# Optimization experiments

Hardware: AMD Instinct MI355X
Metric: run time of the kernel (lower is better)

Reference implementation:

```python
import jax, jax.numpy as jnp
import numpy as np
import math

NH, NKV, HD = 8, 1, 128
SOFTCAP = 30.0
ROPE_BASE = 500000.0


def _rope_tables(T, hd, base):
    half = hd // 2
    inv_freq = 1.0 / (base ** (np.arange(half, dtype=np.float32) / half))
    t = np.arange(T, dtype=np.float32)
    ang = np.outer(t, inv_freq)  # [T, half]
    return jnp.asarray(np.cos(ang)), jnp.asarray(np.sin(ang))


def apply_rope(x, cos, sin):
    # x: [B, T, H, hd]; cos/sin: [T, hd//2]
    half = x.shape[-1] // 2
    x1, x2 = x[..., :half], x[..., half:]
    T = x.shape[1]
    c = cos[:T][None, :, None, :]
    s = sin[:T][None, :, None, :]
    return jnp.concatenate([x1 * c - x2 * s, x1 * s + x2 * c], axis=-1)


def setup_inputs() -> dict:
    key = jax.random.key(0)
    ks = jax.random.split(key, 5)
    B, T, D = 4, 2048, 1024
    KD = NKV * HD
    x = jax.random.normal(ks[0], (B, T, D), dtype=jnp.float32)
    Wq = jax.random.normal(ks[1], (D, D), dtype=jnp.float32) * (D ** -0.5)
    Wk = jax.random.normal(ks[2], (KD, D), dtype=jnp.float32) * (D ** -0.5)
    Wv = jax.random.normal(ks[3], (KD, D), dtype=jnp.float32) * (D ** -0.5)
    Wo = jax.random.normal(ks[4], (D, D), dtype=jnp.float32) * (D ** -0.5)
    qk_gain = jnp.full((NH,), 1.5, dtype=jnp.float32)  # qk_gain_init
    cos, sin = _rope_tables(T, HD, ROPE_BASE)
    return {"x": x, "Wq": Wq, "Wk": Wk, "Wv": Wv, "Wo": Wo,
            "qk_gain": qk_gain, "cos": cos, "sin": sin}


def reference(x, Wq, Wk, Wv, Wo, qk_gain, cos, sin):
    B, T, D = x.shape
    # projections (QuantLinear with qat disabled == plain linear, no bias)
    q = (x @ Wq.T).reshape(B, T, NH, HD)
    k = (x @ Wk.T).reshape(B, T, NKV, HD)
    v = (x @ Wv.T).reshape(B, T, NKV, HD)
    q = apply_rope(q, cos, sin)
    k = apply_rope(k, cos, sin)
    # learned per-head QK gain applied to queries
    q = q * qk_gain[None, None, :, 1 - 1][..., None] if False else q * qk_gain[None, None, :, None]
    # GQA: broadcast the single kv head across NH query heads
    scale = 1.0 / math.sqrt(HD)
    scores = jnp.einsum('bqhd,bkgd->bhqk', q, k) * scale  # g==NKV==1 broadcast
    # logit softcap before masking/softmax
    scores = SOFTCAP * jnp.tanh(scores / SOFTCAP)
    causal = jnp.tril(jnp.ones((T, T), dtype=bool))
    scores = jnp.where(causal[None, None], scores, -jnp.inf)
    attn = jax.nn.softmax(scores, axis=-1)  # [B, NH, T, T]
    out = jnp.einsum('bhqk,bkgd->bqhd', attn, v).reshape(B, T, NH * HD)
    return out @ Wo.T
```

## Files before the change

### kernel.cpp

```cpp
#include <hip/hip_runtime.h>
#include <hip/hip_bf16.h>

#define B_ 4
#define T_ 2048
#define D_ 1024
#define NH_ 8
#define HD_ 128

typedef short short8 __attribute__((ext_vector_type(8)));
typedef float floatx4 __attribute__((ext_vector_type(4)));

#if __has_builtin(__builtin_amdgcn_exp2f)
#define EXP2F __builtin_amdgcn_exp2f
#else
#define EXP2F exp2f
#endif
#if __has_builtin(__builtin_amdgcn_rcpf)
#define RCPF __builtin_amdgcn_rcpf
#else
__device__ __forceinline__ float RCPF(float x) { return 1.f / x; }
#endif

#if __has_builtin(__builtin_amdgcn_global_load_lds)
#define G2L(gp, lp)                                                        \
  __builtin_amdgcn_global_load_lds(                                        \
      (const __attribute__((address_space(1))) unsigned int*)(gp),         \
      (__attribute__((address_space(3))) unsigned int*)(lp), 16, 0, 0)
#else
#define G2L(gp, lp) (*(uint4*)(lp) = *(const uint4*)(gp))
#endif

__device__ __forceinline__ unsigned short f2b(float f) {
  union { float fl; unsigned int i; } v; v.fl = f;
  unsigned int r = v.i + 0x7fffu + ((v.i >> 16) & 1u);
  return (unsigned short)(r >> 16);
}
__device__ __forceinline__ unsigned int pack_bf16(float a, float b) {
  unsigned int ua = __float_as_uint(a) + 0x8000u;
  unsigned int ub = __float_as_uint(b) + 0x8000u;
  return (ua >> 16) | (ub & 0xffff0000u);
}
__device__ __forceinline__ float blo(unsigned int u) { return __uint_as_float(u << 16); }
__device__ __forceinline__ float bhi(unsigned int u) { return __uint_as_float(u & 0xffff0000u); }

__global__ __launch_bounds__(256) void cvt_kernel(
    const float* __restrict__ x,  const float* __restrict__ wq,
    const float* __restrict__ wk, const float* __restrict__ wv,
    const float* __restrict__ wo, unsigned short* __restrict__ dst)
{
  size_t i = ((size_t)blockIdx.x * 256 + threadIdx.x) * 8;
  const float* src; size_t off;
  if      (i <  8388608u) { src = x;  off = i; }
  else if (i <  9437184u) { src = wq; off = i - 8388608u; }
  else if (i <  9568256u) { src = wk; off = i - 9437184u; }
  else if (i <  9699328u) { src = wv; off = i - 9568256u; }
  else                    { src = wo; off = i - 9699328u; }
  float4 a = *(const float4*)(src + off);
  float4 b = *(const float4*)(src + off + 4);
  uint4 o;
  o.x = pack_bf16(a.x, a.y); o.y = pack_bf16(a.z, a.w);
  o.z = pack_bf16(b.x, b.y); o.w = pack_bf16(b.z, b.w);
  *(uint4*)(dst + i) = o;
}

template <bool C_F32>
__device__ __forceinline__ void gemm_body_1024(
    const unsigned short* __restrict__ Arow0,
    const unsigned short* __restrict__ Btile,
    void* __restrict__ Cb, int ldC)
{
  __shared__ unsigned short As[128 * 32];
  __shared__ unsigned short Bs[128 * 32];
  const int tid = threadIdx.x;
  const int lane = tid & 63;
  const int w = tid >> 6;
  const int wr = w >> 1, wc = w & 1;
  const int l15 = lane & 15, quad = lane >> 4;

  const unsigned short* a_src = Arow0 + (size_t)(tid >> 2) * 1024 + (tid & 3) * 8;
  const unsigned short* b_src = Btile + (size_t)(tid >> 2) * 1024 + (tid & 3) * 8;
  unsigned short* a_dst = &As[(tid >> 2) * 32 + (tid & 3) * 8];
  unsigned short* b_dst = &Bs[(tid >> 2) * 32 + (tid & 3) * 8];

  floatx4 zero = {0.f, 0.f, 0.f, 0.f};
  floatx4 acc[4][4];
#pragma unroll
  for (int i = 0; i < 4; i++)
#pragma unroll
    for (int j = 0; j < 4; j++) acc[i][j] = zero;

  for (int k0 = 0; k0 < 1024; k0 += 32) {
    __syncthreads();
    G2L(a_src + k0,         a_dst);
    G2L(a_src + 65536 + k0, a_dst + 2048);
    G2L(b_src + k0,         b_dst);
    G2L(b_src + 65536 + k0, b_dst + 2048);
    __syncthreads();
    short8 af[4], bfr[4];
#pragma unroll
    for (int i = 0; i < 4; i++)
      af[i] = *(const short8*)&As[(wr * 64 + i * 16 + l15) * 32 + quad * 8];
#pragma unroll
    for (int j = 0; j < 4; j++)
      bfr[j] = *(const short8*)&Bs[(wc * 64 + j * 16 + l15) * 32 + quad * 8];
#pragma unroll
    for (int i = 0; i < 4; i++)
#pragma unroll
      for (int j = 0; j < 4; j++)
        acc[i][j] = __builtin_amdgcn_mfma_f32_16x16x32_bf16(af[i], bfr[j], acc[i][j], 0, 0, 0);
  }
#pragma unroll
  for (int i = 0; i < 4; i++)
#pragma unroll
    for (int j = 0; j < 4; j++)
#pragma unroll
      for (int r = 0; r < 4; r++) {
        size_t off = (size_t)(wr * 64 + i * 16 + quad * 4 + r) * ldC + wc * 64 + j * 16 + l15;
        if (C_F32) ((float*)Cb)[off] = acc[i][j][r];
        else ((unsigned short*)Cb)[off] = f2b(acc[i][j][r]);
      }
}

__global__ __launch_bounds__(256) void gemm_qkv_kernel(
    const unsigned short* __restrict__ x,
    const unsigned short* __restrict__ Wq,
    const unsigned short* __restrict__ Wk,
    const unsigned short* __restrict__ Wv,
    unsigned short* __restrict__ q,
    unsigned short* __restrict__ k,
    unsigned short* __restrict__ v)
{
  const int bx = blockIdx.x, by = blockIdx.y;
  const unsigned short* Btile;
  unsigned short* C;
  int ldC, col0;
  if (by < 8) { Btile = Wq + (size_t)by * 128 * 1024; C = q; ldC = 1024; col0 = by * 128; }
  else if (by == 8) { Btile = Wk; C = k; ldC = 128; col0 = 0; }
  else { Btile = Wv; C = v; ldC = 128; col0 = 0; }
  gemm_body_1024<false>(x + (size_t)bx * 128 * 1024, Btile,
                        C + (size_t)bx * 128 * ldC + col0, ldC);
}

__global__ __launch_bounds__(256) void gemm_out_kernel(
    const unsigned short* __restrict__ ao,
    const unsigned short* __restrict__ Wo,
    float* __restrict__ out)
{
  const int bx = blockIdx.x, by = blockIdx.y;
  gemm_body_1024<true>(ao + (size_t)bx * 128 * 1024, Wo + (size_t)by * 128 * 1024,
                       out + (size_t)bx * 128 * 1024 + by * 128, 1024);
}

__global__ __launch_bounds__(256) void prep_kernel(
    unsigned short* __restrict__ q,
    unsigned short* __restrict__ k,
    const unsigned short* __restrict__ v,
    unsigned short* __restrict__ vT,
    const float* __restrict__ cosT,
    const float* __restrict__ sinT,
    const float* __restrict__ gain)
{
  __shared__ unsigned short tile[32 * 136];
  const int tid = threadIdx.x;
  if (blockIdx.x < 256) {
    const int b = blockIdx.x >> 6, t0 = (blockIdx.x & 63) * 32;
    for (int u = tid; u < 512; u += 256) {
      int r = u >> 4, c = u & 15;
      *(uint4*)&tile[r * 136 + c * 8] =
          *(const uint4*)(v + ((size_t)(b * T_ + t0 + r)) * 128 + c * 8);
    }
    __syncthreads();
    for (int u = tid; u < 512; u += 256) {
      int d = u >> 2, c = u & 3;
      short8 val;
#pragma unroll
      for (int j = 0; j < 8; j++) val[j] = (short)tile[(c * 8 + j) * 136 + d];
      *(short8*)(vT + ((size_t)(b * 128 + d)) * T_ + t0 + c * 8) = val;
    }
    return;
  }
  int idx = (blockIdx.x - 256) * 256 + tid;
  unsigned short* ptr;
  size_t base;
  int t, j;
  float g;
  if (idx < 524288) {
    j = idx & 7;
    int h = (idx >> 3) & 7;
    int bt = idx >> 6;
    t = bt & (T_ - 1);
    base = (size_t)bt * 1024 + h * 128 + j * 8;
    ptr = q;
    g = gain[h] * 0.0029462782549439484f;
  } else {
    int id = idx - 524288;
    j = id & 7;
    int bt = id >> 3;
    t = bt & (T_ - 1);
    base = (size_t)bt * 128 + j * 8;
    ptr = k;
    g = 1.f;
  }
  float4 ca = *(const float4*)&cosT[t * 64 + j * 8];
  float4 cb = *(const float4*)&cosT[t * 64 + j * 8 + 4];
  float4 sa = *(const float4*)&sinT[t * 64 + j * 8];
  float4 sb = *(const float4*)&sinT[t * 64 + j * 8 + 4];
  uint4 lo = *(const uint4*)(ptr + base);
  uint4 hi = *(const uint4*)(ptr + base + 64);
  uint4 olo, ohi;
  {
    float a0 = blo(lo.x), a1 = bhi(lo.x), b0 = blo(hi.x), b1 = bhi(hi.x);
    olo.x = pack_bf16((a0 * ca.x - b0 * sa.x) * g, (a1 * ca.y - b1 * sa.y) * g);
    ohi.x = pack_bf16((a0 * sa.x + b0 * ca.x) * g, (a1 * sa.y + b1 * ca.y) * g);
  }
  {
    float a0 = blo(lo.y), a1 = bhi(lo.y), b0 = blo(hi.y), b1 = bhi(hi.y);
    olo.y = pack_bf16((a0 * ca.z - b0 * sa.z) * g, (a1 * ca.w - b1 * sa.w) * g);
    ohi.y = pack_bf16((a0 * sa.z + b0 * ca.z) * g, (a1 * sa.w + b1 * ca.w) * g);
  }
  {
    float a0 = blo(lo.z), a1 = bhi(lo.z), b0 = blo(hi.z), b1 = bhi(hi.z);
    olo.z = pack_bf16((a0 * cb.x - b0 * sb.x) * g, (a1 * cb.y - b1 * sb.y) * g);
    ohi.z = pack_bf16((a0 * sb.x + b0 * cb.x) * g, (a1 * sb.y + b1 * cb.y) * g);
  }
  {
    float a0 = blo(lo.w), a1 = bhi(lo.w), b0 = blo(hi.w), b1 = bhi(hi.w);
    olo.w = pack_bf16((a0 * cb.z - b0 * sb.z) * g, (a1 * cb.w - b1 * sb.w) * g);
    ohi.w = pack_bf16((a0 * sb.z + b0 * cb.z) * g, (a1 * sb.w + b1 * cb.w) * g);
  }
  *(uint4*)(ptr + base) = olo;
  *(uint4*)(ptr + base + 64) = ohi;
}

template <int NSPLIT>
__global__ __launch_bounds__(256, 4) void attn_kernel(
    const unsigned short* __restrict__ q,
    const unsigned short* __restrict__ k,
    const unsigned short* __restrict__ vT,
    unsigned short* __restrict__ ao,
    unsigned short* __restrict__ Opart,
    float* __restrict__ lbuf)
{
  __shared__ unsigned short Ks[2][16 * 264];
  __shared__ unsigned short Vts[2][128 * 40];

  const int h = blockIdx.y, b = blockIdx.z;
  const int pr   = blockIdx.x / NSPLIT;
  const int part = blockIdx.x % NSPLIT;
  const int tid = threadIdx.x, lane = tid & 63, w = tid >> 6;
  const int l15 = lane & 15, quad = lane >> 4;

  const unsigned short* ksrc =
      k + (size_t)b * T_ * 128 + (size_t)(tid >> 4) * 128 + (tid & 15) * 8;
  const int koff0 = (tid & 15) * 264 + (tid >> 4) * 8;
  const int koff1 = koff0 + 16 * 8;
  const unsigned short* vsrc =
      vT + (size_t)b * 128 * T_ + (size_t)(tid >> 2) * T_ + (tid & 3) * 8;
  const int voff0 = (tid >> 2) * 40 + (tid & 3) * 8;
  const int voff1 = voff0 + 64 * 40;

  const floatx4 zero = {0.f, 0.f, 0.f, 0.f};

  for (int pass = 0; pass < 2; pass++) {
    const int chunk = pass ? (31 - pr) : pr;
    const int qw = chunk * 64 + w * 16;
    const int seg = (2 * chunk + 2) / NSPLIT;
    const int ktBeg = part * seg, ktEnd = ktBeg + seg;

    short8 qf[4];
    {
      const unsigned short* qrow =
          q + ((size_t)(b * T_ + qw + l15) * NH_ + h) * HD_;
#pragma unroll
      for (int c = 0; c < 4; c++) qf[c] = *(const short8*)(qrow + c * 32 + quad * 8);
    }

    float l_i = 0.f;
    floatx4 acc[8];
#pragma unroll
    for (int d = 0; d < 8; d++) acc[d] = zero;

    __syncthreads();
    {
      uint4 kr0 = *(const uint4*)(ksrc + (size_t)ktBeg * 4096);
      uint4 kr1 = *(const uint4*)(ksrc + (size_t)ktBeg * 4096 + 2048);
      uint4 vr0 = *(const uint4*)(vsrc + ktBeg * 32);
      uint4 vr1 = *(const uint4*)(vsrc + (size_t)64 * T_ + ktBeg * 32);
      unsigned short* kb = Ks[ktBeg & 1];
      unsigned short* vb = Vts[ktBeg & 1];
      *(uint4*)(kb + koff0) = kr0; *(uint4*)(kb + koff1) = kr1;
      *(uint4*)(vb + voff0) = vr0; *(uint4*)(vb + voff1) = vr1;
    }

    for (int kt = ktBeg; kt < ktEnd; kt++) {
      __syncthreads();
      uint4 kr0, kr1, vr0, vr1;
      const bool more = (kt + 1 < ktEnd);
      if (more) {
        kr0 = *(const uint4*)(ksrc + (size_t)(kt + 1) * 4096);
        kr1 = *(const uint4*)(ksrc + (size_t)(kt + 1) * 4096 + 2048);
        vr0 = *(const uint4*)(vsrc + (kt + 1) * 32);
        vr1 = *(const uint4*)(vsrc + (size_t)64 * T_ + (kt + 1) * 32);
      }

      if (kt * 32 <= qw + 15) {
        const unsigned short* KsC = Ks[kt & 1];
        const unsigned short* VtC = Vts[kt & 1];
        floatx4 st[2] = {zero, zero};
#pragma unroll
        for (int c = 0; c < 4; c++) {
          const int dg = (c * 4 + quad) * 264;
          short8 kf0 = *(const short8*)&KsC[dg + l15 * 8];
          short8 kf1 = *(const short8*)&KsC[dg + (16 + l15) * 8];
          st[0] = __builtin_amdgcn_mfma_f32_16x16x32_bf16(kf0, qf[c], st[0], 0, 0, 0);
          st[1] = __builtin_amdgcn_mfma_f32_16x16x32_bf16(kf1, qf[c], st[1], 0, 0, 0);
        }
        float rs = 0.f;
        short8 pf;
        {
          float pv[2][4];
          if (kt * 32 + 31 <= qw) {
#pragma unroll
            for (int f = 0; f < 2; f++)
#pragma unroll
              for (int r = 0; r < 4; r++) {
                float s = st[f][r];
                float e = EXP2F(2.8853901f * s);
                float u = RCPF(e + 1.f);
                float p = EXP2F(-86.561707f * u);
                pv[f][r] = p;
                rs += p;
              }
          } else {
            const int qrow = qw + l15;
#pragma unroll
            for (int f = 0; f < 2; f++)
#pragma unroll
              for (int r = 0; r < 4; r++) {
                float s = st[f][r];
                float e = EXP2F(2.8853901f * s);
                float u = RCPF(e + 1.f);
                float p = EXP2F(-86.561707f * u);
                int key = kt * 32 + f * 16 + quad * 4 + r;
                p = (key <= qrow) ? p : 0.f;
                pv[f][r] = p;
                rs += p;
              }
          }
          unsigned int pa = pack_bf16(pv[0][0], pv[0][1]);
          unsigned int pb = pack_bf16(pv[0][2], pv[0][3]);
          unsigned int pc = pack_bf16(pv[1][0], pv[1][1]);
          unsigned int pd = pack_bf16(pv[1][2], pv[1][3]);
          asm("v_permlane32_swap_b32 %0, %1" : "+v"(pa), "+v"(pc));
          asm("v_permlane32_swap_b32 %0, %1" : "+v"(pb), "+v"(pd));
          asm("v_permlane16_swap_b32 %0, %1" : "+v"(pa), "+v"(pc));
          asm("v_permlane16_swap_b32 %0, %1" : "+v"(pb), "+v"(pd));
          uint4 u; u.x = pa; u.y = pb; u.z = pc; u.w = pd;
          pf = *(short8*)&u;
        }
        {
          float r2 = rs + __shfl_xor(rs, 16);
          l_i += r2 + __shfl_xor(r2, 32);
        }
#pragma unroll
        for (int d = 0; d < 8; d++) {
          short8 vf = *(const short8*)&VtC[(d * 16 + l15) * 40 + quad * 8];
          acc[d] = __builtin_amdgcn_mfma_f32_16x16x32_bf16(vf, pf, acc[d], 0, 0, 0);
        }
      }

      if (more) {
        unsigned short* kb = Ks[(kt + 1) & 1];
        unsigned short* vb = Vts[(kt + 1) & 1];
        *(uint4*)(kb + koff0) = kr0; *(uint4*)(kb + koff1) = kr1;
        *(uint4*)(vb + voff0) = vr0; *(uint4*)(vb + voff1) = vr1;
      }
    }

    {
      const size_t rowidx = (size_t)(b * T_ + qw + l15) * NH_ + h;
      if (NSPLIT == 1) {
        float linv = 1.f / l_i;
        unsigned short* aop = ao + rowidx * HD_ + quad * 4;
#pragma unroll
        for (int d = 0; d < 8; d++) {
          uint2 o;
          o.x = pack_bf16(acc[d][0] * linv, acc[d][1] * linv);
          o.y = pack_bf16(acc[d][2] * linv, acc[d][3] * linv);
          *(uint2*)(aop + d * 16) = o;
        }
      } else {
        unsigned short* dst =
            ((part == NSPLIT - 1) ? ao : Opart + (size_t)part * 8388608u) +
            rowidx * HD_ + quad * 4;
#pragma unroll
        for (int d = 0; d < 8; d++) {
          uint2 o;
          o.x = pack_bf16(acc[d][0], acc[d][1]);
          o.y = pack_bf16(acc[d][2], acc[d][3]);
          *(uint2*)(dst + d * 16) = o;
        }
        if (quad == 0) lbuf[(size_t)part * 65536u + rowidx] = l_i;
      }
    }
  }
}

template <int NSPLIT>
__global__ __launch_bounds__(256) void combine_kernel(
    const unsigned short* __restrict__ Opart,
    const float* __restrict__ lbuf,
    unsigned short* __restrict__ ao)
{
  size_t i = ((size_t)blockIdx.x * 256 + threadIdx.x) * 8;
  size_t r = i >> 7;
  float ls = 0.f;
#pragma unroll
  for (int p = 0; p < NSPLIT; p++) ls += lbuf[(size_t)p * 65536u + r];
  float linv = RCPF(ls);
  uint4 c = *(const uint4*)(ao + i);
  float v0 = blo(c.x), v1 = bhi(c.x), v2 = blo(c.y), v3 = bhi(c.y);
  float v4 = blo(c.z), v5 = bhi(c.z), v6 = blo(c.w), v7 = bhi(c.w);
#pragma unroll
  for (int p = 0; p < NSPLIT - 1; p++) {
    uint4 a = *(const uint4*)(Opart + (size_t)p * 8388608u + i);
    v0 += blo(a.x); v1 += bhi(a.x); v2 += blo(a.y); v3 += bhi(a.y);
    v4 += blo(a.z); v5 += bhi(a.z); v6 += blo(a.w); v7 += bhi(a.w);
  }
  uint4 o;
  o.x = pack_bf16(v0 * linv, v1 * linv);
  o.y = pack_bf16(v2 * linv, v3 * linv);
  o.z = pack_bf16(v4 * linv, v5 * linv);
  o.w = pack_bf16(v6 * linv, v7 * linv);
  *(uint4*)(ao + i) = o;
}

extern "C" void kernel_launch(void* const* d_in, const int* in_sizes, int n_in,
                              void* d_out, int out_size, void* d_ws, size_t ws_size,
                              hipStream_t stream) {
  const float* x    = (const float*)d_in[0];
  const float* Wq   = (const float*)d_in[1];
  const float* Wk   = (const float*)d_in[2];
  const float* Wv   = (const float*)d_in[3];
  const float* Wo   = (const float*)d_in[4];
  const float* gain = (const float*)d_in[5];
  const float* cosT = (const float*)d_in[6];
  const float* sinT = (const float*)d_in[7];
  float* out = (float*)d_out;

  unsigned short* ws = (unsigned short*)d_ws;
  unsigned short* blob = ws;
  unsigned short* xb  = blob;
  unsigned short* Wqb = blob + 8388608u;
  unsigned short* Wkb = blob + 9437184u;
  unsigned short* Wvb = blob + 9568256u;
  unsigned short* Wob = blob + 9699328u;
  unsigned short* q   = ws + 10747904u;
  unsigned short* kk  = ws + 19136512u;
  unsigned short* v   = ws + 20185088u;
  unsigned short* vT  = ws + 21233664u;
  unsigned short* ao  = xb;
  unsigned short* Opart = ws + 22282240u;
  float* l2 = (float*)((char*)d_ws + 61341696u);
  const size_t need2 = 61865984ull;

  cvt_kernel<<<5248, 256, 0, stream>>>(x, Wq, Wk, Wv, Wo, blob);
  gemm_qkv_kernel<<<dim3(64, 10), 256, 0, stream>>>(xb, Wqb, Wkb, Wvb, q, kk, v);
  prep_kernel<<<2560, 256, 0, stream>>>(q, kk, v, vT, cosT, sinT, gain);
  if (ws_size >= need2) {
    attn_kernel<2><<<dim3(32, 8, 4), 256, 0, stream>>>(q, kk, vT, ao, Opart, l2);
    combine_kernel<2><<<4096, 256, 0, stream>>>(Opart, l2, ao);
  } else {
    attn_kernel<1><<<dim3(16, 8, 4), 256, 0, stream>>>(q, kk, vT, ao, Opart, l2);
  }
  gemm_out_kernel<<<dim3(64, 8), 256, 0, stream>>>(ao, Wob, out);
}
```

Baseline: 234.3 us.

## Switch attention to 32x32x16 MFMA tiles with 128-row query blocks and 3-way split

Attention now uses 32x32x16 bf16 MFMA instructions, with each wave owning 32 query rows, so each block covers 128 queries instead of 64. The goal is better reuse of K/V reads from LDS per MFMA and fewer permlane shuffles and reductions. The key range is split three ways when enough workspace is available, with a remainder-aware split and a matching 3-way combine. In exchange, register pressure rises (launch bounds drop from 4 to 3 waves) and the combine step handles a third partial buffer.

```diff
diff --git a/kernel.cpp b/kernel.cpp
--- a/kernel.cpp
+++ b/kernel.cpp
@@ -9,6 +9,7 @@
 
 typedef short short8 __attribute__((ext_vector_type(8)));
 typedef float floatx4 __attribute__((ext_vector_type(4)));
+typedef float floatx16 __attribute__((ext_vector_type(16)));
 
 #if __has_builtin(__builtin_amdgcn_exp2f)
 #define EXP2F __builtin_amdgcn_exp2f
@@ -233,7 +234,7 @@
 }
 
 template <int NSPLIT>
-__global__ __launch_bounds__(256, 4) void attn_kernel(
+__global__ __launch_bounds__(256, 3) void attn_kernel(
     const unsigned short* __restrict__ q,
     const unsigned short* __restrict__ k,
     const unsigned short* __restrict__ vT,
@@ -248,7 +249,7 @@
   const int pr   = blockIdx.x / NSPLIT;
   const int part = blockIdx.x % NSPLIT;
   const int tid = threadIdx.x, lane = tid & 63, w = tid >> 6;
-  const int l15 = lane & 15, quad = lane >> 4;
+  const int q32 = lane & 31, hi = lane >> 5;
 
   const unsigned short* ksrc =
       k + (size_t)b * T_ * 128 + (size_t)(tid >> 4) * 128 + (tid & 15) * 8;
@@ -259,26 +260,28 @@
   const int voff0 = (tid >> 2) * 40 + (tid & 3) * 8;
   const int voff1 = voff0 + 64 * 40;
 
-  const floatx4 zero = {0.f, 0.f, 0.f, 0.f};
-
   for (int pass = 0; pass < 2; pass++) {
-    const int chunk = pass ? (31 - pr) : pr;
-    const int qw = chunk * 64 + w * 16;
-    const int seg = (2 * chunk + 2) / NSPLIT;
-    const int ktBeg = part * seg, ktEnd = ktBeg + seg;
-
-    short8 qf[4];
+    const int qblock = pass ? (15 - pr) : pr;
+    const int qw = qblock * 128 + w * 32;
+    const int nkt = 4 * qblock + 4;
+    const int base = nkt / NSPLIT, rem = nkt % NSPLIT;
+    const int ktBeg = part * base + (part < rem ? part : rem);
+    const int ktEnd = ktBeg + base + (part < rem ? 1 : 0);
+
+    short8 qf[8];
     {
       const unsigned short* qrow =
-          q + ((size_t)(b * T_ + qw + l15) * NH_ + h) * HD_;
-#pragma unroll
-      for (int c = 0; c < 4; c++) qf[c] = *(const short8*)(qrow + c * 32 + quad * 8);
+          q + ((size_t)(b * T_ + qw + q32) * NH_ + h) * HD_ + hi * 8;
+#pragma unroll
+      for (int c = 0; c < 8; c++) qf[c] = *(const short8*)(qrow + c * 16);
     }
 
     float l_i = 0.f;
-    floatx4 acc[8];
-#pragma unroll
-    for (int d = 0; d < 8; d++) acc[d] = zero;
+    floatx16 acc[4];
+#pragma unroll
+    for (int dt = 0; dt < 4; dt++)
+#pragma unroll
+      for (int r = 0; r < 16; r++) acc[dt][r] = 0.f;
 
     __syncthreads();
     {
@@ -303,69 +306,66 @@
         vr1 = *(const uint4*)(vsrc + (size_t)64 * T_ + (kt + 1) * 32);
       }
 
-      if (kt * 32 <= qw + 15) {
+      if (kt * 32 <= qw + 31) {
         const unsigned short* KsC = Ks[kt & 1];
         const unsigned short* VtC = Vts[kt & 1];
-        floatx4 st[2] = {zero, zero};
-#pragma unroll
-        for (int c = 0; c < 4; c++) {
-          const int dg = (c * 4 + quad) * 264;
-          short8 kf0 = *(const short8*)&KsC[dg + l15 * 8];
-          short8 kf1 = *(const short8*)&KsC[dg + (16 + l15) * 8];
-          st[0] = __builtin_amdgcn_mfma_f32_16x16x32_bf16(kf0, qf[c], st[0], 0, 0, 0);
-          st[1] = __builtin_amdgcn_mfma_f32_16x16x32_bf16(kf1, qf[c], st[1], 0, 0, 0);
+        floatx16 st;
+#pragma unroll
+        for (int r = 0; r < 16; r++) st[r] = 0.f;
+#pragma unroll
+        for (int c = 0; c < 8; c++) {
+          short8 kf = *(const short8*)&KsC[(2 * c + hi) * 264 + q32 * 8];
+          st = __builtin_amdgcn_mfma_f32_32x32x16_bf16(kf, qf[c], st, 0, 0, 0);
         }
         float rs = 0.f;
-        short8 pf;
-        {
-          float pv[2][4];
-          if (kt * 32 + 31 <= qw) {
-#pragma unroll
-            for (int f = 0; f < 2; f++)
-#pragma unroll
-              for (int r = 0; r < 4; r++) {
-                float s = st[f][r];
-                float e = EXP2F(2.8853901f * s);
-                float u = RCPF(e + 1.f);
-                float p = EXP2F(-86.561707f * u);
-                pv[f][r] = p;
-                rs += p;
-              }
-          } else {
-            const int qrow = qw + l15;
-#pragma unroll
-            for (int f = 0; f < 2; f++)
-#pragma unroll
-              for (int r = 0; r < 4; r++) {
-                float s = st[f][r];
-                float e = EXP2F(2.8853901f * s);
-                float u = RCPF(e + 1.f);
-                float p = EXP2F(-86.561707f * u);
-                int key = kt * 32 + f * 16 + quad * 4 + r;
-                p = (key <= qrow) ? p : 0.f;
-                pv[f][r] = p;
-                rs += p;
-              }
+        unsigned int A[8];
+        if (kt * 32 + 31 <= qw) {
+          float pv[16];
+#pragma unroll
+          for (int r = 0; r < 16; r++) {
+            float s = st[r];
+            float e = EXP2F(2.8853901f * s);
+            float u = RCPF(e + 1.f);
+            float p = EXP2F(-86.561707f * u);
+            pv[r] = p;
+            rs += p;
           }
-          unsigned int pa = pack_bf16(pv[0][0], pv[0][1]);
-          unsigned int pb = pack_bf16(pv[0][2], pv[0][3]);
-          unsigned int pc = pack_bf16(pv[1][0], pv[1][1]);
-          unsigned int pd = pack_bf16(pv[1][2], pv[1][3]);
-          asm("v_permlane32_swap_b32 %0, %1" : "+v"(pa), "+v"(pc));
-          asm("v_permlane32_swap_b32 %0, %1" : "+v"(pb), "+v"(pd));
-          asm("v_permlane16_swap_b32 %0, %1" : "+v"(pa), "+v"(pc));
-          asm("v_permlane16_swap_b32 %0, %1" : "+v"(pb), "+v"(pd));
-          uint4 u; u.x = pa; u.y = pb; u.z = pc; u.w = pd;
-          pf = *(short8*)&u;
+#pragma unroll
+          for (int m = 0; m < 8; m++) A[m] = pack_bf16(pv[2 * m], pv[2 * m + 1]);
+        } else {
+          const int qrow = qw + q32;
+          float pv[16];
+#pragma unroll
+          for (int r = 0; r < 16; r++) {
+            float s = st[r];
+            float e = EXP2F(2.8853901f * s);
+            float u = RCPF(e + 1.f);
+            float p = EXP2F(-86.561707f * u);
+            int key = kt * 32 + (r & 3) + 8 * (r >> 2) + 4 * hi;
+            p = (key <= qrow) ? p : 0.f;
+            pv[r] = p;
+            rs += p;
+          }
+#pragma unroll
+          for (int m = 0; m < 8; m++) A[m] = pack_bf16(pv[2 * m], pv[2 * m + 1]);
         }
-        {
-          float r2 = rs + __shfl_xor(rs, 16);
-          l_i += r2 + __shfl_xor(r2, 32);
-        }
-#pragma unroll
-        for (int d = 0; d < 8; d++) {
-          short8 vf = *(const short8*)&VtC[(d * 16 + l15) * 40 + quad * 8];
-          acc[d] = __builtin_amdgcn_mfma_f32_16x16x32_bf16(vf, pf, acc[d], 0, 0, 0);
+        unsigned int a0 = A[0], a1 = A[1], a2 = A[2], a3 = A[3];
+        unsigned int a4 = A[4], a5 = A[5], a6 = A[6], a7 = A[7];
+        asm("v_permlane32_swap_b32 %0, %1" : "+v"(a0), "+v"(a2));
+        asm("v_permlane32_swap_b32 %0, %1" : "+v"(a1), "+v"(a3));
+        asm("v_permlane32_swap_b32 %0, %1" : "+v"(a4), "+v"(a6));
+        asm("v_permlane32_swap_b32 %0, %1" : "+v"(a5), "+v"(a7));
+        uint4 u0; u0.x = a0; u0.y = a1; u0.z = a2; u0.w = a3;
+        uint4 u1; u1.x = a4; u1.y = a5; u1.z = a6; u1.w = a7;
+        short8 pf0 = *(short8*)&u0;
+        short8 pf1 = *(short8*)&u1;
+        l_i += rs + __shfl_xor(rs, 32);
+#pragma unroll
+        for (int dt = 0; dt < 4; dt++) {
+          short8 v0 = *(const short8*)&VtC[(dt * 32 + q32) * 40 + hi * 8];
+          short8 v1 = *(const short8*)&VtC[(dt * 32 + q32) * 40 + 16 + hi * 8];
+          acc[dt] = __builtin_amdgcn_mfma_f32_32x32x16_bf16(v0, pf0, acc[dt], 0, 0, 0);
+          acc[dt] = __builtin_amdgcn_mfma_f32_32x32x16_bf16(v1, pf1, acc[dt], 0, 0, 0);
         }
       }
 
@@ -378,29 +378,33 @@
     }
 
     {
-      const size_t rowidx = (size_t)(b * T_ + qw + l15) * NH_ + h;
+      const size_t rowidx = (size_t)(b * T_ + qw + q32) * NH_ + h;
       if (NSPLIT == 1) {
         float linv = 1.f / l_i;
-        unsigned short* aop = ao + rowidx * HD_ + quad * 4;
-#pragma unroll
-        for (int d = 0; d < 8; d++) {
-          uint2 o;
-          o.x = pack_bf16(acc[d][0] * linv, acc[d][1] * linv);
-          o.y = pack_bf16(acc[d][2] * linv, acc[d][3] * linv);
-          *(uint2*)(aop + d * 16) = o;
-        }
+        unsigned short* aop = ao + rowidx * HD_;
+#pragma unroll
+        for (int dt = 0; dt < 4; dt++)
+#pragma unroll
+          for (int rg = 0; rg < 4; rg++) {
+            uint2 o;
+            o.x = pack_bf16(acc[dt][4 * rg + 0] * linv, acc[dt][4 * rg + 1] * linv);
+            o.y = pack_bf16(acc[dt][4 * rg + 2] * linv, acc[dt][4 * rg + 3] * linv);
+            *(uint2*)(aop + dt * 32 + rg * 8 + hi * 4) = o;
+          }
       } else {
         unsigned short* dst =
             ((part == NSPLIT - 1) ? ao : Opart + (size_t)part * 8388608u) +
-            rowidx * HD_ + quad * 4;
-#pragma unroll
-        for (int d = 0; d < 8; d++) {
-          uint2 o;
-          o.x = pack_bf16(acc[d][0], acc[d][1]);
-          o.y = pack_bf16(acc[d][2], acc[d][3]);
-          *(uint2*)(dst + d * 16) = o;
-        }
-        if (quad == 0) lbuf[(size_t)part * 65536u + rowidx] = l_i;
+            rowidx * HD_;
+#pragma unroll
+        for (int dt = 0; dt < 4; dt++)
+#pragma unroll
+          for (int rg = 0; rg < 4; rg++) {
+            uint2 o;
+            o.x = pack_bf16(acc[dt][4 * rg + 0], acc[dt][4 * rg + 1]);
+            o.y = pack_bf16(acc[dt][4 * rg + 2], acc[dt][4 * rg + 3]);
+            *(uint2*)(dst + dt * 32 + rg * 8 + hi * 4) = o;
+          }
+        if (hi == 0) lbuf[(size_t)part * 65536u + rowidx] = l_i;
       }
     }
   }
@@ -463,15 +467,20 @@
   unsigned short* Opart = ws + 22282240u;
   float* l2 = (float*)((char*)d_ws + 61341696u);
   const size_t need2 = 61865984ull;
+  float* l3 = (float*)((char*)d_ws + 78118912u);
+  const size_t need3 = 78905344ull;
 
   cvt_kernel<<<5248, 256, 0, stream>>>(x, Wq, Wk, Wv, Wo, blob);
   gemm_qkv_kernel<<<dim3(64, 10), 256, 0, stream>>>(xb, Wqb, Wkb, Wvb, q, kk, v);
   prep_kernel<<<2560, 256, 0, stream>>>(q, kk, v, vT, cosT, sinT, gain);
-  if (ws_size >= need2) {
-    attn_kernel<2><<<dim3(32, 8, 4), 256, 0, stream>>>(q, kk, vT, ao, Opart, l2);
+  if (ws_size >= need3) {
+    attn_kernel<3><<<dim3(24, 8, 4), 256, 0, stream>>>(q, kk, vT, ao, Opart, l3);
+    combine_kernel<3><<<4096, 256, 0, stream>>>(Opart, l3, ao);
+  } else if (ws_size >= need2) {
+    attn_kernel<2><<<dim3(16, 8, 4), 256, 0, stream>>>(q, kk, vT, ao, Opart, l2);
     combine_kernel<2><<<4096, 256, 0, stream>>>(Opart, l2, ao);
   } else {
-    attn_kernel<1><<<dim3(16, 8, 4), 256, 0, stream>>>(q, kk, vT, ao, Opart, l2);
+    attn_kernel<1><<<dim3(8, 8, 4), 256, 0, stream>>>(q, kk, vT, ao, Opart, l2);
   }
   gemm_out_kernel<<<dim3(64, 8), 256, 0, stream>>>(ao, Wob, out);
 }
```

Result: no change. 234.0 us (-0.1%).
